# Performance work log

Measured on AMD Instinct MI355X. Metric: run time of the kernel, lower is better.

Reference implementation:

```python
import jax, jax.numpy as jnp
import numpy as np

DS_STEPS = 9
MAX_RND = 1.0
SMOKE_AUG = 0.5
SIZE = 512


def diamond_square(key, steps=DS_STEPS, max_rnd=MAX_RND):
    """Vectorized, faithful port of f_seed_grid + f_dsmain.

    Notes on faithfulness to the original code:
      - interior 'temp' reads in the diamond step resolve to the cell's own
        center (i_min + half == i_mid), exactly as in the original (buggy)
        indexing, so the interior averages double-count the center.
      - the '== 0' guards mean top/left edge midpoints are only written for
        the first row/column of cells (fresh zeros); elsewhere they were
        already written as bottom/right edges of neighboring cells.
    All per-level updates read only square-step (center) and coarser-level
    values, so each level is fully parallel.
    """
    N = 2 ** steps + 1
    hm = jnp.zeros((N, N), jnp.float32)
    corners = jax.random.uniform(jax.random.fold_in(key, 1000), (4,), minval=-1.0, maxval=1.0)
    hm = (hm.at[0, 0].set(corners[0]).at[0, -1].set(corners[1])
            .at[-1, 0].set(corners[2]).at[-1, -1].set(corners[3]))
    L = N - 1  # shape_length
    for level in range(steps):
        g = 2 ** level          # grid_split
        h = L // 2              # half_v_grid_size
        r = max_rnd / (level + 1)
        ks = jax.random.split(jax.random.fold_in(key, level), 5)
        lows = jnp.arange(g) * L
        highs = lows + L
        mids = lows + h
        # corner reads (set at coarser levels / seeds)
        nw = hm[lows[:, None], lows[None, :]]
        ne = hm[lows[:, None], highs[None, :]]
        sw = hm[highs[:, None], lows[None, :]]
        se = hm[highs[:, None], highs[None, :]]
        # square step: cell centers
        centers = (nw + ne + sw + se) / 4.0 + jax.random.uniform(ks[0], (g, g), minval=-r, maxval=r)
        hm = hm.at[mids[:, None], mids[None, :]].set(centers)
        # diamond step (all reads from post-square values)
        # top row (only i_min==0 cells pass the ==0 guard); temp = hm[max_index-h, j_mid] = centers[g-1, j]
        top = (centers[0, :] + hm[0, lows] + hm[0, highs] + centers[g - 1, :]) / 4.0 \
              + jax.random.uniform(ks[1], (g,), minval=-r, maxval=r)
        # left col (only j_min==0 cells); temp = hm[i_mid, max_index-h] = centers[i, g-1]
        left = (centers[:, 0] + hm[lows, 0] + hm[highs, 0] + centers[:, g - 1]) / 4.0 \
               + jax.random.uniform(ks[2], (g,), minval=-r, maxval=r)
        # right edges of every cell; interior temp == own center, boundary temp = centers[i, 0]
        temp_r = jnp.where(jnp.arange(g)[None, :] < g - 1, centers, centers[:, :1])
        right = (centers + ne + se + temp_r) / 4.0 + jax.random.uniform(ks[3], (g, g), minval=-r, maxval=r)
        # bottom edges of every cell; interior temp == own center, boundary temp = centers[0, j]
        temp_b = jnp.where(jnp.arange(g)[:, None] < g - 1, centers, centers[:1, :])
        bottom = (centers + sw + se + temp_b) / 4.0 + jax.random.uniform(ks[4], (g, g), minval=-r, maxval=r)
        hm = hm.at[0, mids].set(top)
        hm = hm.at[mids, 0].set(left)
        hm = hm.at[mids[:, None], highs[None, :]].set(right)
        hm = hm.at[highs[:, None], mids[None, :]].set(bottom)
        L //= 2
    return hm


def make_smoke_noise(key):
    hm = diamond_square(key)
    noise = (hm - hm.min()) / (hm.max() - hm.min())          # [513, 513] in [0,1]
    noise = jax.image.resize(noise, (SIZE, SIZE), method="bilinear")
    return noise * SMOKE_AUG                                  # [H, W]


def setup_inputs() -> dict:
    key = jax.random.key(0)
    img = jax.random.uniform(key, (32, 3, 512, 512), dtype=jnp.float32)
    return {"img": img}


def reference(img) -> jnp.ndarray:
    rn = make_smoke_noise(jax.random.key(42))                 # [H, W]
    rn = rn[None, None]                                       # broadcast over [B, C, H, W]
    return jnp.clip(img * (1.0 - rn) + rn, 0.0, 1.0)
```

## Files before the change

### kernel.cpp

```cpp
#include <hip/hip_runtime.h>

struct KP { unsigned a, b; };

__host__ __device__ constexpr unsigned rotl32(unsigned x, int d) {
  return (x << d) | (x >> (32 - d));
}

__host__ __device__ constexpr KP tf2x32(unsigned k0, unsigned k1, unsigned x0, unsigned x1) {
  unsigned k2 = k0 ^ k1 ^ 0x1BD11BDAu;
  unsigned v0 = x0 + k0;
  unsigned v1 = x1 + k1;
  const int R[5][4] = {{13,15,26,6},{17,29,16,24},{13,15,26,6},{17,29,16,24},{13,15,26,6}};
  const unsigned KI[5][2] = {{k1, k2 + 1u},{k2, k0 + 2u},{k0, k1 + 3u},{k1, k2 + 4u},{k2, k0 + 5u}};
  for (int g = 0; g < 5; ++g) {
    for (int r = 0; r < 4; ++r) {
      v0 += v1;
      v1 = rotl32(v1, R[g][r]);
      v1 ^= v0;
    }
    v0 += KI[g][0];
    v1 += KI[g][1];
  }
  return KP{v0, v1};
}

struct AllKeys {
  unsigned lk[9][5][2];
  unsigned ck[2];
};

__host__ __device__ constexpr AllKeys make_keys() {
  AllKeys K{};
  for (int l = 0; l < 9; ++l) {
    KP base = tf2x32(0u, 42u, 0u, (unsigned)l);
    for (int m = 0; m < 5; ++m) {
      KP s = tf2x32(base.a, base.b, 0u, (unsigned)m);
      K.lk[l][m][0] = s.a;
      K.lk[l][m][1] = s.b;
    }
  }
  KP ck = tf2x32(0u, 42u, 0u, 1000u);
  K.ck[0] = ck.a;
  K.ck[1] = ck.b;
  return K;
}

constexpr AllKeys KEYS = make_keys();

#define NG 513

__device__ inline unsigned rbits(unsigned k0, unsigned k1, unsigned i) {
  KP o = tf2x32(k0, k1, 0u, i);
  return o.a ^ o.b;
}

__device__ inline float bits_to_u(unsigned b, float r) {
  float u = __uint_as_float((b >> 9) | 0x3f800000u) - 1.0f;
  return fmaxf(-r, u * (2.0f * r) - r);
}

__device__ inline float draw_u(const unsigned* kk, unsigned i, float r) {
  return bits_to_u(rbits(kk[0], kk[1], i), r);
}

__device__ inline unsigned enc_f(float f) {
  unsigned u = __float_as_uint(f);
  return (u & 0x80000000u) ? ~u : (u | 0x80000000u);
}
__device__ inline float dec_f(unsigned e) {
  unsigned u = (e & 0x80000000u) ? (e & 0x7FFFFFFFu) : ~e;
  return __uint_as_float(u);
}

__device__ inline float cell_center(const float* hm, int level, int g, int L,
                                    int a, int b, float r) {
  int lo_i = a * L, hi_i = lo_i + L, lo_j = b * L, hi_j = lo_j + L;
  float nw = hm[lo_i * NG + lo_j], ne = hm[lo_i * NG + hi_j];
  float sw = hm[hi_i * NG + lo_j], se = hm[hi_i * NG + hi_j];
  return (nw + ne + sw + se) * 0.25f +
         draw_u(KEYS.lk[level][0], (unsigned)(a * g + b), r);
}

__device__ inline void do_cell(float* hm, int level, int i, int j,
                               float& mn, float& mx) {
  int g = 1 << level;
  int L = 512 >> level;
  int h = L >> 1;
  float r = 1.0f / (float)(level + 1);
  int lo_i = i * L, hi_i = lo_i + L, mi_i = lo_i + h;
  int lo_j = j * L, hi_j = lo_j + L, mi_j = lo_j + h;
  float nw = hm[lo_i * NG + lo_j], ne = hm[lo_i * NG + hi_j];
  float sw = hm[hi_i * NG + lo_j], se = hm[hi_i * NG + hi_j];
  unsigned m = (unsigned)(i * g + j);

  float c = (nw + ne + sw + se) * 0.25f + draw_u(KEYS.lk[level][0], m, r);
  hm[mi_i * NG + mi_j] = c;
  mn = fminf(mn, c); mx = fmaxf(mx, c);

  float tr = (j < g - 1) ? c : cell_center(hm, level, g, L, i, 0, r);
  float right = (c + ne + se + tr) * 0.25f + draw_u(KEYS.lk[level][3], m, r);
  hm[mi_i * NG + hi_j] = right;
  mn = fminf(mn, right); mx = fmaxf(mx, right);

  float tb = (i < g - 1) ? c : cell_center(hm, level, g, L, 0, j, r);
  float bottom = (c + sw + se + tb) * 0.25f + draw_u(KEYS.lk[level][4], m, r);
  hm[hi_i * NG + mi_j] = bottom;
  mn = fminf(mn, bottom); mx = fmaxf(mx, bottom);

  if (i == 0) {
    float cg1 = (g == 1) ? c : cell_center(hm, level, g, L, g - 1, j, r);
    float top = (c + hm[lo_j] + hm[hi_j] + cg1) * 0.25f +
                draw_u(KEYS.lk[level][1], (unsigned)j, r);
    hm[mi_j] = top;
    mn = fminf(mn, top); mx = fmaxf(mx, top);
  }
  if (j == 0) {
    float cg1 = (g == 1) ? c : cell_center(hm, level, g, L, i, g - 1, r);
    float left = (c + hm[lo_i * NG] + hm[hi_i * NG] + cg1) * 0.25f +
                 draw_u(KEYS.lk[level][2], (unsigned)i, r);
    hm[mi_i * NG] = left;
    mn = fminf(mn, left); mx = fmaxf(mx, left);
  }
}

template <int NWAVES>
__device__ inline void block_minmax_atomic(float mn, float mx, unsigned* mmx) {
  __shared__ float smn[NWAVES], smx[NWAVES];
#pragma unroll
  for (int off = 32; off >= 1; off >>= 1) {
    mn = fminf(mn, __shfl_down(mn, off, 64));
    mx = fmaxf(mx, __shfl_down(mx, off, 64));
  }
  int lane = threadIdx.x & 63, w = threadIdx.x >> 6;
  if (lane == 0) { smn[w] = mn; smx[w] = mx; }
  __syncthreads();
  if (threadIdx.x == 0) {
#pragma unroll
    for (int q = 1; q < NWAVES; ++q) {
      mn = fminf(mn, smn[q]);
      mx = fmaxf(mx, smx[q]);
    }
    atomicMin(&mmx[0], enc_f(mn));
    atomicMax(&mmx[1], enc_f(mx));
  }
}

__global__ void k_ds_small(float* hm, unsigned* mmx) {
  int tid = threadIdx.x;
  float mn = 3.4e38f, mx = -3.4e38f;
  if (tid == 0) {
    mmx[0] = 0xFFFFFFFFu;
    mmx[1] = 0u;
  }
  if (tid < 4) {
    float v = bits_to_u(rbits(KEYS.ck[0], KEYS.ck[1], (unsigned)tid), 1.0f);
    int y = (tid >> 1) ? 512 : 0;
    int x = (tid & 1) ? 512 : 0;
    hm[y * NG + x] = v;
    mn = fminf(mn, v); mx = fmaxf(mx, v);
  }
  __syncthreads();
  for (int lvl = 0; lvl <= 5; ++lvl) {
    int g = 1 << lvl;
    if (tid < g * g) do_cell(hm, lvl, tid >> lvl, tid & (g - 1), mn, mx);
    __syncthreads();
  }
  for (int c = tid; c < 64 * 64; c += 1024)
    do_cell(hm, 6, c >> 6, c & 63, mn, mx);
  block_minmax_atomic<16>(mn, mx, mmx);
}

__global__ void k_level(float* hm, unsigned* mmx, int level) {
  int g = 1 << level;
  int gt = blockIdx.x * blockDim.x + threadIdx.x;
  float mn = 3.4e38f, mx = -3.4e38f;
  do_cell(hm, level, gt >> level, gt & (g - 1), mn, mx);
  block_minmax_atomic<4>(mn, mx, mmx);
}

__global__ void k_apply(const float4* __restrict__ img, const float* __restrict__ hm,
                        const unsigned* __restrict__ mmx, float4* __restrict__ out) {
  int t = blockIdx.x * blockDim.x + threadIdx.x;
  int pos4 = t & (512 * 512 / 4 - 1);
  int oy = pos4 >> 7;
  int ox = (pos4 & 127) << 2;

  float mn = dec_f(mmx[0]);
  float scale = 0.5f / (dec_f(mmx[1]) - mn);

  const float csc = 512.0f / 513.0f;
  float dy = (float)(2 * oy + 1) * (1.0f / 1024.0f);
  float wy0 = 1.0f - dy * csc;
  float wy1 = 1.0f - (1.0f - dy) * csc;
  float sy = wy0 + wy1;
  wy0 /= sy; wy1 /= sy;

  const float* r0 = hm + oy * NG + ox;
  float n[4];
#pragma unroll
  for (int k = 0; k < 4; ++k) {
    float dx = (float)(2 * (ox + k) + 1) * (1.0f / 1024.0f);
    float wx0 = 1.0f - dx * csc;
    float wx1 = 1.0f - (1.0f - dx) * csc;
    float sx = wx0 + wx1;
    wx0 /= sx; wx1 /= sx;
    float v = wy0 * (wx0 * r0[k] + wx1 * r0[k + 1]) +
              wy1 * (wx0 * r0[NG + k] + wx1 * r0[NG + k + 1]);
    n[k] = (v - mn) * scale;
  }

  float4 a = img[t];
  float4 o;
  o.x = fminf(fmaxf(a.x * (1.0f - n[0]) + n[0], 0.0f), 1.0f);
  o.y = fminf(fmaxf(a.y * (1.0f - n[1]) + n[1], 0.0f), 1.0f);
  o.z = fminf(fmaxf(a.z * (1.0f - n[2]) + n[2], 0.0f), 1.0f);
  o.w = fminf(fmaxf(a.w * (1.0f - n[3]) + n[3], 0.0f), 1.0f);
  out[t] = o;
}

extern "C" void kernel_launch(void* const* d_in, const int* in_sizes, int n_in,
                              void* d_out, int out_size, void* d_ws, size_t ws_size,
                              hipStream_t stream) {
  const float* img = (const float*)d_in[0];
  float* out = (float*)d_out;
  unsigned char* ws = (unsigned char*)d_ws;

  unsigned* mmx = (unsigned*)ws;
  float* hm = (float*)(ws + 16);

  hipLaunchKernelGGL(k_ds_small, dim3(1), dim3(1024), 0, stream, hm, mmx);
  hipLaunchKernelGGL(k_level, dim3(64), dim3(256), 0, stream, hm, mmx, 7);
  hipLaunchKernelGGL(k_level, dim3(256), dim3(256), 0, stream, hm, mmx, 8);

  const int total = 32 * 3 * 512 * 512;
  hipLaunchKernelGGL(k_apply, dim3(total / 4 / 256), dim3(256), 0, stream,
                     (const float4*)img, hm, mmx, (float4*)out);
}
```

Before: 227.5 us.

## Precompute noise map once, stream image with nontemporal loads/stores

Splits the bilinear resize and normalization into a separate k_noise kernel that writes a 512x512 noise buffer to workspace once. The apply kernel then only reads a float4 of noise per image float4, uses nontemporal loads and stores for the image and output, and handles two elements per thread. This removes the per-pixel bilinear arithmetic and heightmap gathers that were repeated for all 96 image planes. It adds one extra kernel launch and a 1 MB intermediate buffer.

```diff
diff --git a/kernel.cpp b/kernel.cpp
--- a/kernel.cpp
+++ b/kernel.cpp
@@ -178,44 +178,47 @@
   block_minmax_atomic<4>(mn, mx, mmx);
 }
 
-__global__ void k_apply(const float4* __restrict__ img, const float* __restrict__ hm,
-                        const unsigned* __restrict__ mmx, float4* __restrict__ out) {
-  int t = blockIdx.x * blockDim.x + threadIdx.x;
-  int pos4 = t & (512 * 512 / 4 - 1);
-  int oy = pos4 >> 7;
-  int ox = (pos4 & 127) << 2;
-
-  float mn = dec_f(mmx[0]);
-  float scale = 0.5f / (dec_f(mmx[1]) - mn);
-
+__global__ void k_noise(const float* __restrict__ hm, const unsigned* __restrict__ mmx,
+                        float* __restrict__ rn) {
+  int o = blockIdx.x * blockDim.x + threadIdx.x;
+  int oy = o >> 9, ox = o & 511;
   const float csc = 512.0f / 513.0f;
+  float dx = (float)(2 * ox + 1) * (1.0f / 1024.0f);
+  float wx0 = 1.0f - dx * csc;
+  float wx1 = 1.0f - (1.0f - dx) * csc;
+  float sx = wx0 + wx1;
+  wx0 /= sx; wx1 /= sx;
   float dy = (float)(2 * oy + 1) * (1.0f / 1024.0f);
   float wy0 = 1.0f - dy * csc;
   float wy1 = 1.0f - (1.0f - dy) * csc;
   float sy = wy0 + wy1;
   wy0 /= sy; wy1 /= sy;
-
   const float* r0 = hm + oy * NG + ox;
-  float n[4];
+  float v = wy0 * (wx0 * r0[0] + wx1 * r0[1]) + wy1 * (wx0 * r0[NG] + wx1 * r0[NG + 1]);
+  float mn = dec_f(mmx[0]), mx = dec_f(mmx[1]);
+  rn[o] = 0.5f * ((v - mn) / (mx - mn));
+}
+
+typedef float vf4 __attribute__((ext_vector_type(4)));
+
+#define TOTAL4 (32 * 3 * 512 * 512 / 4)
+__global__ __launch_bounds__(256) void k_apply(const vf4* __restrict__ img,
+                                               const vf4* __restrict__ rn,
+                                               vf4* __restrict__ out) {
+  int t = blockIdx.x * blockDim.x + threadIdx.x;
 #pragma unroll
-  for (int k = 0; k < 4; ++k) {
-    float dx = (float)(2 * (ox + k) + 1) * (1.0f / 1024.0f);
-    float wx0 = 1.0f - dx * csc;
-    float wx1 = 1.0f - (1.0f - dx) * csc;
-    float sx = wx0 + wx1;
-    wx0 /= sx; wx1 /= sx;
-    float v = wy0 * (wx0 * r0[k] + wx1 * r0[k + 1]) +
-              wy1 * (wx0 * r0[NG + k] + wx1 * r0[NG + k + 1]);
-    n[k] = (v - mn) * scale;
-  }
-
-  float4 a = img[t];
-  float4 o;
-  o.x = fminf(fmaxf(a.x * (1.0f - n[0]) + n[0], 0.0f), 1.0f);
-  o.y = fminf(fmaxf(a.y * (1.0f - n[1]) + n[1], 0.0f), 1.0f);
-  o.z = fminf(fmaxf(a.z * (1.0f - n[2]) + n[2], 0.0f), 1.0f);
-  o.w = fminf(fmaxf(a.w * (1.0f - n[3]) + n[3], 0.0f), 1.0f);
-  out[t] = o;
+  for (int rep = 0; rep < 2; ++rep) {
+    int idx = t + rep * (TOTAL4 / 2);
+    int pos4 = idx & (512 * 512 / 4 - 1);
+    vf4 a = __builtin_nontemporal_load(&img[idx]);
+    vf4 n = rn[pos4];
+    vf4 o;
+    o.x = fminf(fmaxf(a.x * (1.0f - n.x) + n.x, 0.0f), 1.0f);
+    o.y = fminf(fmaxf(a.y * (1.0f - n.y) + n.y, 0.0f), 1.0f);
+    o.z = fminf(fmaxf(a.z * (1.0f - n.z) + n.z, 0.0f), 1.0f);
+    o.w = fminf(fmaxf(a.w * (1.0f - n.w) + n.w, 0.0f), 1.0f);
+    __builtin_nontemporal_store(o, &out[idx]);
+  }
 }
 
 extern "C" void kernel_launch(void* const* d_in, const int* in_sizes, int n_in,
@@ -225,14 +228,15 @@
   float* out = (float*)d_out;
   unsigned char* ws = (unsigned char*)d_ws;
 
+  const size_t RN_BYTES = 512 * 512 * sizeof(float);
   unsigned* mmx = (unsigned*)ws;
-  float* hm = (float*)(ws + 16);
+  float* rn = (float*)(ws + 16);
+  float* hm = (float*)(ws + 16 + RN_BYTES);
 
   hipLaunchKernelGGL(k_ds_small, dim3(1), dim3(1024), 0, stream, hm, mmx);
   hipLaunchKernelGGL(k_level, dim3(64), dim3(256), 0, stream, hm, mmx, 7);
   hipLaunchKernelGGL(k_level, dim3(256), dim3(256), 0, stream, hm, mmx, 8);
-
-  const int total = 32 * 3 * 512 * 512;
-  hipLaunchKernelGGL(k_apply, dim3(total / 4 / 256), dim3(256), 0, stream,
-                     (const float4*)img, hm, mmx, (float4*)out);
-}
+  hipLaunchKernelGGL(k_noise, dim3(512 * 512 / 256), dim3(256), 0, stream, hm, mmx, rn);
+  hipLaunchKernelGGL(k_apply, dim3(TOTAL4 / 2 / 256), dim3(256), 0, stream,
+                     (const vf4*)img, (const vf4*)rn, (vf4*)out);
+}
```

After: 223.8 us. Within noise of the previous version (-1.6%).
